# Optimization experiments

Measured on AMD Instinct MI355X. Metric: run time of the kernel, lower is better.

## Reference

```python
import jax, jax.numpy as jnp
import numpy as np

K = 2  # top-k routing (init kwarg k=2)


def setup_inputs() -> dict:
    key = jax.random.key(0)
    k1, k2 = jax.random.split(key)
    in_flow = jax.random.normal(k1, (8192, 2048), dtype=jnp.float32)
    gates = jax.random.uniform(k2, (8192, 8), dtype=jnp.float32)
    return {"in_flow": in_flow, "gates": gates}


def reference(in_flow, gates):
    # in_flow: [N, D] tokens; gates: [N, E]
    N, E = gates.shape
    # --- gen_indices (topk branch): one-hot-k routing mask [N, E] ---
    top_idx = jax.lax.top_k(gates, K)[1]                       # [N, K]
    mask = jnp.zeros((N, E), dtype=jnp.int32)
    mask = mask.at[jnp.arange(N)[:, None], top_idx].set(1)     # scatter_(1, idx, 1)
    # --- dispatch: per-expert gather, concatenated expert-major ---
    # torch.nonzero(mask.T[i]) returns token indices ascending per expert;
    # stable argsort of expert-major flattened mask reproduces exactly that
    # concatenation order, and topk guarantees exactly N*K selected rows.
    flat = mask.T.reshape(-1)                                  # [E*N], expert-major
    order = jnp.argsort(-flat)                                 # stable: ones first, in order
    sel = order[: N * K]                                       # flat positions of assignments
    token_idx = sel % N                                        # [N*K] source token per row
    out_data = in_flow[token_idx]                              # [N*K, D] routed flow
    out_tags = token_idx                                       # tags (pack_invalid_flow arange tags)
    counts = mask.sum(axis=0)                                  # [E] rows per destination (loads)
    return out_data, out_tags, counts
```

## Files before the change

kernel.cpp:

```cpp
#include <hip/hip_runtime.h>
#include <hip/hip_bf16.h>


#define EXPERTS 8
#define TOPK 2
#define N_TOK 8192
#define NK (N_TOK * TOPK)
#define RT_THREADS 1024
#define TOK_PER_THR (N_TOK / RT_THREADS)
#define RT_WAVES (RT_THREADS / 64)

__global__ __launch_bounds__(RT_THREADS) void k_route(
        const float* __restrict__ gates,
        int* __restrict__ tok_of_pos,
        float* __restrict__ out_tags,
        float* __restrict__ counts_out) {
    const int t    = threadIdx.x;
    const int wave = t >> 6;
    const int lane = t & 63;

    int mask[TOK_PER_THR];
    int cnt[EXPERTS];
    #pragma unroll
    for (int e = 0; e < EXPERTS; e++) cnt[e] = 0;

    const float4* g4 = (const float4*)gates;
    #pragma unroll
    for (int k = 0; k < TOK_PER_THR; k++) {
        int n = t * TOK_PER_THR + k;
        float4 a = g4[2 * n], b = g4[2 * n + 1];
        float v[EXPERTS] = {a.x, a.y, a.z, a.w, b.x, b.y, b.z, b.w};
        int e1 = 0; float b1 = v[0];
        #pragma unroll
        for (int e = 1; e < EXPERTS; e++) if (v[e] > b1) { b1 = v[e]; e1 = e; }
        int e2 = -1; float b2 = -1e30f;
        #pragma unroll
        for (int e = 0; e < EXPERTS; e++) if (e != e1 && v[e] > b2) { b2 = v[e]; e2 = e; }
        mask[k] = (1 << e1) | (1 << e2);
        cnt[e1]++; cnt[e2]++;
    }

    int pk[4], incl[4];
    #pragma unroll
    for (int j = 0; j < 4; j++) pk[j] = cnt[2 * j] | (cnt[2 * j + 1] << 16);

    #pragma unroll
    for (int j = 0; j < 4; j++) incl[j] = pk[j];
    #pragma unroll
    for (int d = 1; d < 64; d <<= 1) {
        #pragma unroll
        for (int j = 0; j < 4; j++) {
            int up = __shfl_up(incl[j], d, 64);
            if (lane >= d) incl[j] += up;
        }
    }

    __shared__ int wtot[RT_WAVES][4];
    if (lane == 63) {
        #pragma unroll
        for (int j = 0; j < 4; j++) wtot[wave][j] = incl[j];
    }
    __syncthreads();
    int wpref[4], tot[4];
    #pragma unroll
    for (int j = 0; j < 4; j++) { wpref[j] = 0; tot[j] = 0; }
    for (int w = 0; w < RT_WAVES; w++) {
        #pragma unroll
        for (int j = 0; j < 4; j++) {
            int x = wtot[w][j];
            if (w < wave) wpref[j] += x;
            tot[j] += x;
        }
    }

    int tote[EXPERTS], base[EXPERTS];
    #pragma unroll
    for (int j = 0; j < 4; j++) {
        tote[2 * j]     = tot[j] & 0xFFFF;
        tote[2 * j + 1] = (tot[j] >> 16) & 0xFFFF;
    }
    int acc = 0;
    #pragma unroll
    for (int e = 0; e < EXPERTS; e++) { base[e] = acc; acc += tote[e]; }

    int rank[EXPERTS];
    #pragma unroll
    for (int j = 0; j < 4; j++) {
        int excl = incl[j] - pk[j];
        rank[2 * j]     = base[2 * j]     + ((wpref[j] + excl) & 0xFFFF);
        rank[2 * j + 1] = base[2 * j + 1] + (((wpref[j] + excl) >> 16) & 0xFFFF);
    }

    #pragma unroll
    for (int k = 0; k < TOK_PER_THR; k++) {
        int n = t * TOK_PER_THR + k;
        int m = mask[k];
        #pragma unroll
        for (int e = 0; e < EXPERTS; e++) {
            if ((m >> e) & 1) {
                int pos = rank[e]++;
                tok_of_pos[pos] = n;
                out_tags[pos] = (float)n;
            }
        }
    }

    if (t < EXPERTS) counts_out[t] = (float)tote[t];
}

#define CP_BLOCKS 2048
#define CP_THREADS 256

__global__ __launch_bounds__(CP_THREADS) void k_copy(
        const float* __restrict__ in_flow,
        const int* __restrict__ tok_of_pos,
        float* __restrict__ out_data, int D) {
    const int lane   = threadIdx.x & 63;
    const int wid    = blockIdx.x * (CP_THREADS / 64) + (threadIdx.x >> 6);
    const int nwaves = CP_BLOCKS * (CP_THREADS / 64);

    for (int p = wid; p < NK; p += nwaves) {
        int tok = tok_of_pos[p];
        const float4* src = (const float4*)(in_flow + (size_t)tok * D);
        float4*       dst = (float4*)(out_data + (size_t)p * D);
        float4 r[8];
        #pragma unroll
        for (int i = 0; i < 8; i++) r[i] = src[lane + 64 * i];
        #pragma unroll
        for (int i = 0; i < 8; i++) dst[lane + 64 * i] = r[i];
    }
}

extern "C" void kernel_launch(void* const* d_in, const int* in_sizes, int n_in,
                              void* d_out, int out_size, void* d_ws, size_t ws_size,
                              hipStream_t stream) {
    const float* in_flow = (const float*)d_in[0];
    const float* gates   = (const float*)d_in[1];
    const int D = in_sizes[0] / N_TOK;

    int* tok_of_pos = (int*)d_ws;

    float* out_data   = (float*)d_out;
    float* out_tags   = out_data + (size_t)NK * D;
    float* counts_out = out_tags + NK;

    hipLaunchKernelGGL(k_route, dim3(1), dim3(RT_THREADS), 0, stream,
                       gates, tok_of_pos, out_tags, counts_out);
    hipLaunchKernelGGL(k_copy, dim3(CP_BLOCKS), dim3(CP_THREADS), 0, stream,
                       in_flow, tok_of_pos, out_data, D);
}
```

Measured before the change: 209.7 us.

## Scatter each token row to both expert slots instead of gathering per output row

Result: faster. 203.4 us (-3.0%).

```diff
diff --git a/kernel.cpp b/kernel.cpp
--- a/kernel.cpp
+++ b/kernel.cpp
@@ -12,8 +12,7 @@
 
 __global__ __launch_bounds__(RT_THREADS) void k_route(
         const float* __restrict__ gates,
-        int* __restrict__ tok_of_pos,
-        float* __restrict__ out_tags,
+        int2* __restrict__ pos_pair,
         float* __restrict__ counts_out) {
     const int t    = threadIdx.x;
     const int wave = t >> 6;
@@ -95,40 +94,44 @@
     for (int k = 0; k < TOK_PER_THR; k++) {
         int n = t * TOK_PER_THR + k;
         int m = mask[k];
+        int p[2]; int idx = 0;
         #pragma unroll
         for (int e = 0; e < EXPERTS; e++) {
-            if ((m >> e) & 1) {
-                int pos = rank[e]++;
-                tok_of_pos[pos] = n;
-                out_tags[pos] = (float)n;
-            }
+            if ((m >> e) & 1) p[idx++] = rank[e]++;
         }
+        pos_pair[n] = make_int2(p[0], p[1]);
     }
 
     if (t < EXPERTS) counts_out[t] = (float)tote[t];
 }
 
-#define CP_BLOCKS 2048
 #define CP_THREADS 256
+#define CP_BLOCKS (N_TOK / (CP_THREADS / 64))
 
 __global__ __launch_bounds__(CP_THREADS) void k_copy(
         const float* __restrict__ in_flow,
-        const int* __restrict__ tok_of_pos,
-        float* __restrict__ out_data, int D) {
-    const int lane   = threadIdx.x & 63;
-    const int wid    = blockIdx.x * (CP_THREADS / 64) + (threadIdx.x >> 6);
-    const int nwaves = CP_BLOCKS * (CP_THREADS / 64);
+        const int2* __restrict__ pos_pair,
+        float* __restrict__ out_data,
+        float* __restrict__ out_tags, int D) {
+    const int lane = threadIdx.x & 63;
+    const int n    = blockIdx.x * (CP_THREADS / 64) + (threadIdx.x >> 6);
 
-    for (int p = wid; p < NK; p += nwaves) {
-        int tok = tok_of_pos[p];
-        const float4* src = (const float4*)(in_flow + (size_t)tok * D);
-        float4*       dst = (float4*)(out_data + (size_t)p * D);
-        float4 r[8];
-        #pragma unroll
-        for (int i = 0; i < 8; i++) r[i] = src[lane + 64 * i];
-        #pragma unroll
-        for (int i = 0; i < 8; i++) dst[lane + 64 * i] = r[i];
-    }
+    int2 pp = pos_pair[n];
+
+    const float4* src = (const float4*)(in_flow + (size_t)n * D);
+    float4 r[8];
+    #pragma unroll
+    for (int i = 0; i < 8; i++) r[i] = src[lane + 64 * i];
+
+    float4* dst1 = (float4*)(out_data + (size_t)pp.x * D);
+    float4* dst2 = (float4*)(out_data + (size_t)pp.y * D);
+    #pragma unroll
+    for (int i = 0; i < 8; i++) dst1[lane + 64 * i] = r[i];
+    #pragma unroll
+    for (int i = 0; i < 8; i++) dst2[lane + 64 * i] = r[i];
+
+    if (lane == 0) out_tags[pp.x] = (float)n;
+    if (lane == 1) out_tags[pp.y] = (float)n;
 }
 
 extern "C" void kernel_launch(void* const* d_in, const int* in_sizes, int n_in,
@@ -138,14 +141,14 @@
     const float* gates   = (const float*)d_in[1];
     const int D = in_sizes[0] / N_TOK;
 
-    int* tok_of_pos = (int*)d_ws;
+    int2* pos_pair = (int2*)d_ws;
 
     float* out_data   = (float*)d_out;
     float* out_tags   = out_data + (size_t)NK * D;
     float* counts_out = out_tags + NK;
 
     hipLaunchKernelGGL(k_route, dim3(1), dim3(RT_THREADS), 0, stream,
-                       gates, tok_of_pos, out_tags, counts_out);
+                       gates, pos_pair, counts_out);
     hipLaunchKernelGGL(k_copy, dim3(CP_BLOCKS), dim3(CP_THREADS), 0, stream,
-                       in_flow, tok_of_pos, out_data, D);
+                       in_flow, pos_pair, out_data, out_tags, D);
 }
```
